# Performance work log

Hardware: AMD Instinct MI355X
Metric: run time of the kernel (lower is better)

Reference implementation:

```python
import jax, jax.numpy as jnp
import numpy as np

L, B, T, D, V = 2, 16, 20, 768, 30000


def setup_inputs() -> dict:
    key = jax.random.key(0)
    k1, k2, k3, k4 = jax.random.split(key, 4)
    answer_embed = jax.random.normal(k1, (L, B, T, D), dtype=jnp.float32)
    vocab_embed = 0.1 * jax.random.normal(k2, (V, D), dtype=jnp.float32)
    # classifier_transform modeled as Linear(D, D): y = x @ W.T + b
    W = jax.random.normal(k3, (D, D), dtype=jnp.float32) * (1.0 / np.sqrt(D))
    b = jax.random.normal(k4, (D,), dtype=jnp.float32) * 0.01
    return {"answer_embed": answer_embed, "vocab_embed": vocab_embed, "W": W, "b": b}


def reference(answer_embed, vocab_embed, W, b):
    # vocab_classifiers: [V, D] after the linear transform
    vocab_classifiers = vocab_embed @ W.T + b
    # Original: broadcast multiply [L,B,T,D,1]*[1,1,1,D,V] then sum over D.
    # Mathematically identical contraction over D -> [L, B, T, V]
    return jnp.einsum('lbtd,vd->lbtv', answer_embed, vocab_classifiers)
```

## Files before the change

### kernel.cpp

```cpp
#include <hip/hip_runtime.h>

#define KDIM 768
#define MANS 640
#define VV   30000
#define NGRP 235
#define NKS  (KDIM / 64)
#define VELEM (VV * KDIM)
#define CVTBLK ((VELEM + 8191) / 8192)
#define A2BLK  ((MANS / 64) * (KDIM / 128))

typedef __attribute__((ext_vector_type(4)))  float  f32x4;
typedef __attribute__((ext_vector_type(16))) float  f32x16;
typedef __attribute__((ext_vector_type(8)))  __bf16 bf16x8;
typedef __attribute__((ext_vector_type(8)))  unsigned short ushort8;

__device__ __forceinline__ unsigned short f2bf(float f) {
    union { __bf16 h; unsigned short u; } t;
    t.h = (__bf16)f;
    return t.u;
}

__device__ __forceinline__ ushort8 cvt8(f32x4 a, f32x4 b) {
    union { bf16x8 h; ushort8 u; } c;
    c.h[0] = (__bf16)a.x; c.h[1] = (__bf16)a.y;
    c.h[2] = (__bf16)a.z; c.h[3] = (__bf16)a.w;
    c.h[4] = (__bf16)b.x; c.h[5] = (__bf16)b.y;
    c.h[6] = (__bf16)b.z; c.h[7] = (__bf16)b.w;
    return c.u;
}

__device__ __forceinline__ void load_lds16(const unsigned short* g, unsigned short* l) {
    __builtin_amdgcn_global_load_lds(
        (__attribute__((address_space(1))) void*)(void*)g,
        (__attribute__((address_space(3))) void*)l,
        16, 0, 0);
}

__device__ __forceinline__ long a2f_off(int m, int n) {
    int mb = m >> 7, wm = (m >> 6) & 1, fm = (m >> 5) & 1, colm = m & 31;
    int kt = n >> 6, g = (n >> 4) & 3, halfb = (n >> 3) & 1, e = n & 7;
    return ((((long)(mb * 12 + kt) * 2 + wm) * 2 + fm) * 4 + g) * 512
         + (halfb * 32 + colm) * 8 + e;
}

__global__ __launch_bounds__(256) void prep_small(
    const float* __restrict__ W, const float* __restrict__ A,
    const float* __restrict__ b, unsigned short* __restrict__ Wt_bf,
    float* __restrict__ cvec)
{
    __shared__ float ts[64][65];
    const int blk = blockIdx.x;
    if (blk < 144) {
        int bx = (blk % 12) * 64, by = (blk / 12) * 64;
        int tx = threadIdx.x & 63, tg = threadIdx.x >> 6;
#pragma unroll
        for (int i = 0; i < 16; ++i) {
            int r = tg * 16 + i;
            ts[r][tx] = W[(long)(by + r) * KDIM + bx + tx];
        }
        __syncthreads();
#pragma unroll
        for (int i = 0; i < 16; ++i) {
            int r = tg * 16 + i;
            Wt_bf[(long)(bx + r) * KDIM + by + tx] = f2bf(ts[tx][r]);
        }
    } else {
        int row  = (blk - 144) * 4 + (threadIdx.x >> 6);
        int lane = threadIdx.x & 63;
        const float* ap = A + (long)row * KDIM;
        float s = 0.f;
#pragma unroll
        for (int i = 0; i < KDIM / 64; ++i) s += ap[i * 64 + lane] * b[i * 64 + lane];
#pragma unroll
        for (int off = 32; off; off >>= 1) s += __shfl_down(s, off, 64);
        if (lane == 0) cvec[row] = s;
    }
}

__global__ __launch_bounds__(256) void gemm_a2(
    const float* __restrict__ Af, const unsigned short* __restrict__ Bp,
    unsigned short* __restrict__ outp,
    const float* __restrict__ vocab, unsigned short* __restrict__ vocab_bf)
{
    if (blockIdx.x >= A2BLK) {
        const long base = (long)(blockIdx.x - A2BLK) * 8192 + (long)threadIdx.x * 8;
#pragma unroll
        for (int p = 0; p < 4; ++p) {
            long idx = base + p * 2048;
            if (idx < VELEM) {
                f32x4 v0 = ((const f32x4*)(vocab + idx))[0];
                f32x4 v1 = ((const f32x4*)(vocab + idx))[1];
                *(ushort8*)(vocab_bf + idx) = cvt8(v0, v1);
            }
        }
        return;
    }

    constexpr int TM = 64, TN = 128;
    __shared__ unsigned short sA[TM * 64];
    __shared__ unsigned short sB[TN * 64];

    const int t    = threadIdx.x;
    const int lane = t & 63;
    const int w    = t >> 6;
    const int wm   = w >> 1;
    const int wn   = w & 1;
    const int half = lane >> 5;
    const int col  = lane & 31;
    const long m0  = (long)(blockIdx.x % (MANS / 64)) * TM;
    const long n0  = (long)(blockIdx.x / (MANS / 64)) * TN;

    f32x16 acc[2];
    acc[0] = (f32x16)(0.f);
    acc[1] = (f32x16)(0.f);

    const float* gaf[2]; int laOff[2];
#pragma unroll
    for (int j = 0; j < 2; ++j) {
        int s   = (j * 4 + w) * 64 + lane;
        int row = s >> 3;
        int c   = (s & 7) ^ (row & 7);
        gaf[j]   = Af + (m0 + row) * KDIM + c * 8;
        laOff[j] = s * 8;
    }
    const unsigned short* gb[4]; unsigned short* lbB[4];
#pragma unroll
    for (int j = 0; j < 4; ++j) {
        int s   = (j * 4 + w) * 64 + lane;
        int row = s >> 3;
        int c   = (s & 7) ^ (row & 7);
        gb[j]  = Bp + (n0 + row) * KDIM + c * 8;
        lbB[j] = &sB[(j * 4 + w) * 64 * 8];
    }

    for (int k0 = 0; k0 < KDIM; k0 += 64) {
#pragma unroll
        for (int j = 0; j < 4; ++j) load_lds16(gb[j] + k0, lbB[j]);
#pragma unroll
        for (int j = 0; j < 2; ++j) {
            f32x4 v0 = ((const f32x4*)(gaf[j] + k0))[0];
            f32x4 v1 = ((const f32x4*)(gaf[j] + k0))[1];
            *(ushort8*)(&sA[0] + laOff[j]) = cvt8(v0, v1);
        }
        __syncthreads();

#pragma unroll
        for (int g = 0; g < 4; ++g) {
            const int cg = g * 2 + half;
            int arow = wm * 32 + col;
            bf16x8 af = *(const bf16x8*)&sA[(arow * 8 + (cg ^ (arow & 7))) * 8];
#pragma unroll
            for (int fn = 0; fn < 2; ++fn) {
                int brow = wn * 64 + fn * 32 + col;
                bf16x8 bfv = *(const bf16x8*)&sB[(brow * 8 + (cg ^ (brow & 7))) * 8];
                acc[fn] = __builtin_amdgcn_mfma_f32_32x32x16_bf16(
                    af, bfv, acc[fn], 0, 0, 0);
            }
        }
        __syncthreads();
    }

#pragma unroll
    for (int fn = 0; fn < 2; ++fn) {
        int n = (int)n0 + wn * 64 + fn * 32 + col;
#pragma unroll
        for (int rg = 0; rg < 16; ++rg) {
            int m = (int)m0 + wm * 32 + (rg & 3) + 8 * (rg >> 2) + 4 * half;
            outp[a2f_off(m, n)] = f2bf(acc[fn][rg]);
        }
    }
}

__global__ __launch_bounds__(256, 4) void gemm_big(
    const unsigned short* __restrict__ A, const unsigned short* __restrict__ Bbf,
    const float* __restrict__ cvec, float* __restrict__ outp)
{
    const int id    = blockIdx.x;
    const int x     = id & 7;
    const int q     = id >> 3;
    const int m_idx = q % 5;
    const int n_grp = (q / 5) * 8 + x;
    if (n_grp >= NGRP) return;

    __shared__ unsigned short sB[2][128 * 64];

    const int t    = threadIdx.x;
    const int lane = t & 63;
    const int w    = t >> 6;
    const int wm   = w >> 1;
    const int wn   = w & 1;
    const int half = lane >> 5;
    const int col  = lane & 31;
    const long n0  = (long)n_grp * 128;

    f32x16 acc[2][2];
#pragma unroll
    for (int i = 0; i < 2; ++i)
#pragma unroll
        for (int j = 0; j < 2; ++j) acc[i][j] = (f32x16)(0.f);

    const unsigned short* aBase = A + (((long)(m_idx * 12) * 2 + wm) * 2) * 4 * 512
                                    + lane * 8;

    const unsigned short* gb[4];
    int lbOff[4];
#pragma unroll
    for (int j = 0; j < 4; ++j) {
        int s   = (j * 4 + w) * 64 + lane;
        int row = s >> 3;
        int c   = (s & 7) ^ (row & 7);
        long grow = n0 + row;
        if (grow > VV - 1) grow = VV - 1;
        gb[j]    = Bbf + grow * KDIM + c * 8;
        lbOff[j] = (j * 4 + w) * 64 * 8;
    }

#pragma unroll
    for (int j = 0; j < 4; ++j) load_lds16(gb[j], &sB[0][0] + lbOff[j]);
    asm volatile("s_waitcnt vmcnt(0)" ::: "memory");
    __builtin_amdgcn_s_barrier();

    for (int kt = 0; kt < NKS; ++kt) {
        const int p = kt & 1;
        const unsigned short* aK = aBase + (long)kt * 8192;
        bf16x8 af[2][4];
#pragma unroll
        for (int fm = 0; fm < 2; ++fm)
#pragma unroll
            for (int g = 0; g < 4; ++g)
                af[fm][g] = *(const bf16x8*)(aK + fm * 2048 + g * 512);
        __builtin_amdgcn_sched_barrier(0);
        if (kt < NKS - 1) {
#pragma unroll
            for (int j = 0; j < 4; ++j)
                load_lds16(gb[j] + (kt + 1) * 64,
                           &sB[0][0] + (p ^ 1) * (128 * 64) + lbOff[j]);
        }
        __builtin_amdgcn_sched_barrier(0);
        const unsigned short* bB = &sB[0][0] + p * (128 * 64);
#pragma unroll
        for (int g = 0; g < 4; ++g) {
            const int cg = g * 2 + half;
            bf16x8 bfr[2];
#pragma unroll
            for (int fn = 0; fn < 2; ++fn) {
                int row = wn * 64 + fn * 32 + col;
                bfr[fn] = *(const bf16x8*)&bB[(row * 8 + (cg ^ (row & 7))) * 8];
            }
#pragma unroll
            for (int fm = 0; fm < 2; ++fm)
#pragma unroll
                for (int fn = 0; fn < 2; ++fn)
                    acc[fm][fn] = __builtin_amdgcn_mfma_f32_32x32x16_bf16(
                        af[fm][g], bfr[fn], acc[fm][fn], 0, 0, 0);
        }
        if (kt < NKS - 1) {
            asm volatile("s_waitcnt vmcnt(0)" ::: "memory");
            __builtin_amdgcn_s_barrier();
        }
    }

    const long m0 = (long)m_idx * 128;
#pragma unroll
    for (int fm = 0; fm < 2; ++fm)
#pragma unroll
        for (int fn = 0; fn < 2; ++fn) {
            long n = n0 + wn * 64 + fn * 32 + col;
            if (n < VV) {
#pragma unroll
                for (int rg = 0; rg < 16; ++rg) {
                    long m = m0 + wm * 64 + fm * 32
                           + (rg & 3) + 8 * (rg >> 2) + 4 * half;
                    outp[m * (long)VV + n] = acc[fm][fn][rg] + cvec[m];
                }
            }
        }
}

extern "C" void kernel_launch(void* const* d_in, const int* in_sizes, int n_in,
                              void* d_out, int out_size, void* d_ws, size_t ws_size,
                              hipStream_t stream) {
    const float* answer = (const float*)d_in[0];
    const float* vocab  = (const float*)d_in[1];
    const float* W      = (const float*)d_in[2];
    const float* bvec   = (const float*)d_in[3];

    char* ws = (char*)d_ws;
    unsigned short* Wt_bf   = (unsigned short*)ws;
    unsigned short* A2F     = (unsigned short*)(ws + 1179648);
    float*          cptr    = (float*)(ws + 1179648 + 983040);
    unsigned short* vocabbf = (unsigned short*)(ws + 2165248);

    prep_small<<<304, 256, 0, stream>>>(W, answer, bvec, Wt_bf, cptr);

    gemm_a2<<<A2BLK + CVTBLK, 256, 0, stream>>>(answer, Wt_bf, A2F, vocab, vocabbf);

    gemm_big<<<1200, 256, 0, stream>>>(A2F, vocabbf, cptr, (float*)d_out);
}
```

Before: 221.6 us.

## Keep full-K vocab panel in LDS and loop all M tiles per block

The big GEMM now uses 512-thread blocks, each owning a 64-column slice of the vocab matrix. Each block loads that slice's whole K=768 panel into LDS once and then iterates over all five 128-row M tiles, instead of one block per (M,N) tile with double-buffered K streaming. This reads the large vocab operand from global memory once instead of once per M tile and removes the per-k-step barriers. In exchange, the block uses 96KB of LDS, which limits occupancy. The 64x128 output tile per block also lowers MFMA reuse per LDS load, and A-fragments are read straight from global memory with no prefetch.

```diff
diff --git a/kernel.cpp b/kernel.cpp
--- a/kernel.cpp
+++ b/kernel.cpp
@@ -3,8 +3,8 @@
 #define KDIM 768
 #define MANS 640
 #define VV   30000
-#define NGRP 235
 #define NKS  (KDIM / 64)
+#define NBLK 469
 #define VELEM (VV * KDIM)
 #define CVTBLK ((VELEM + 8191) / 8192)
 #define A2BLK  ((MANS / 64) * (KDIM / 128))
@@ -171,18 +171,11 @@
     }
 }
 
-__global__ __launch_bounds__(256, 4) void gemm_big(
+__global__ __launch_bounds__(512) void gemm_big(
     const unsigned short* __restrict__ A, const unsigned short* __restrict__ Bbf,
     const float* __restrict__ cvec, float* __restrict__ outp)
 {
-    const int id    = blockIdx.x;
-    const int x     = id & 7;
-    const int q     = id >> 3;
-    const int m_idx = q % 5;
-    const int n_grp = (q / 5) * 8 + x;
-    if (n_grp >= NGRP) return;
-
-    __shared__ unsigned short sB[2][128 * 64];
+    __shared__ unsigned short panel[NKS * 4096];
 
     const int t    = threadIdx.x;
     const int lane = t & 63;
@@ -191,90 +184,61 @@
     const int wn   = w & 1;
     const int half = lane >> 5;
     const int col  = lane & 31;
-    const long n0  = (long)n_grp * 128;
-
-    f32x16 acc[2][2];
-#pragma unroll
-    for (int i = 0; i < 2; ++i)
-#pragma unroll
-        for (int j = 0; j < 2; ++j) acc[i][j] = (f32x16)(0.f);
-
-    const unsigned short* aBase = A + (((long)(m_idx * 12) * 2 + wm) * 2) * 4 * 512
-                                    + lane * 8;
-
-    const unsigned short* gb[4];
-    int lbOff[4];
-#pragma unroll
-    for (int j = 0; j < 4; ++j) {
-        int s   = (j * 4 + w) * 64 + lane;
-        int row = s >> 3;
-        int c   = (s & 7) ^ (row & 7);
-        long grow = n0 + row;
-        if (grow > VV - 1) grow = VV - 1;
-        gb[j]    = Bbf + grow * KDIM + c * 8;
-        lbOff[j] = (j * 4 + w) * 64 * 8;
-    }
-
-#pragma unroll
-    for (int j = 0; j < 4; ++j) load_lds16(gb[j], &sB[0][0] + lbOff[j]);
-    asm volatile("s_waitcnt vmcnt(0)" ::: "memory");
-    __builtin_amdgcn_s_barrier();
-
-    for (int kt = 0; kt < NKS; ++kt) {
-        const int p = kt & 1;
-        const unsigned short* aK = aBase + (long)kt * 8192;
-        bf16x8 af[2][4];
-#pragma unroll
-        for (int fm = 0; fm < 2; ++fm)
-#pragma unroll
-            for (int g = 0; g < 4; ++g)
-                af[fm][g] = *(const bf16x8*)(aK + fm * 2048 + g * 512);
-        __builtin_amdgcn_sched_barrier(0);
-        if (kt < NKS - 1) {
-#pragma unroll
-            for (int j = 0; j < 4; ++j)
-                load_lds16(gb[j] + (kt + 1) * 64,
-                           &sB[0][0] + (p ^ 1) * (128 * 64) + lbOff[j]);
-        }
-        __builtin_amdgcn_sched_barrier(0);
-        const unsigned short* bB = &sB[0][0] + p * (128 * 64);
-#pragma unroll
-        for (int g = 0; g < 4; ++g) {
-            const int cg = g * 2 + half;
-            bf16x8 bfr[2];
-#pragma unroll
-            for (int fn = 0; fn < 2; ++fn) {
-                int row = wn * 64 + fn * 32 + col;
-                bfr[fn] = *(const bf16x8*)&bB[(row * 8 + (cg ^ (row & 7))) * 8];
+    const long n0  = (long)blockIdx.x * 64;
+
+    {
+        int row   = t >> 3;
+        int c     = (t & 7) ^ (row & 7);
+        long grow = n0 + row; if (grow > VV - 1) grow = VV - 1;
+        const unsigned short* src = Bbf + grow * KDIM + c * 8;
+        unsigned short*       dst = panel + w * 512;
+#pragma unroll
+        for (int kt = 0; kt < NKS; ++kt)
+            load_lds16(src + kt * 64, dst + kt * 4096);
+    }
+    __syncthreads();
+
+    const int brow = wn * 32 + col;
+    int boff[4];
+#pragma unroll
+    for (int g = 0; g < 4; ++g)
+        boff[g] = (brow * 8 + (((g * 2 + half)) ^ (brow & 7))) * 8;
+
+    const long nstore = n0 + wn * 32 + col;
+    const bool nok    = (nstore < VV);
+
+#pragma unroll 1
+    for (int m_idx = 0; m_idx < 5; ++m_idx) {
+        f32x16 acc0 = (f32x16)(0.f), acc1 = (f32x16)(0.f);
+        const unsigned short* aM = A + ((long)(16 * (m_idx * 12) + 4 * wm)) * 512
+                                     + lane * 8;
+#pragma unroll
+        for (int kt = 0; kt < NKS; ++kt) {
+            const unsigned short* aK = aM + (long)kt * (16 * 512);
+            const unsigned short* pk = panel + kt * 4096;
+            bf16x8 af0 = *(const bf16x8*)(aK + 0 * 512);
+            bf16x8 af1 = *(const bf16x8*)(aK + 1 * 512);
+            bf16x8 af2 = *(const bf16x8*)(aK + 2 * 512);
+            bf16x8 af3 = *(const bf16x8*)(aK + 3 * 512);
+            bf16x8 b0  = *(const bf16x8*)(pk + boff[0]);
+            bf16x8 b1  = *(const bf16x8*)(pk + boff[1]);
+            bf16x8 b2  = *(const bf16x8*)(pk + boff[2]);
+            bf16x8 b3  = *(const bf16x8*)(pk + boff[3]);
+            acc0 = __builtin_amdgcn_mfma_f32_32x32x16_bf16(af0, b0, acc0, 0, 0, 0);
+            acc1 = __builtin_amdgcn_mfma_f32_32x32x16_bf16(af1, b1, acc1, 0, 0, 0);
+            acc0 = __builtin_amdgcn_mfma_f32_32x32x16_bf16(af2, b2, acc0, 0, 0, 0);
+            acc1 = __builtin_amdgcn_mfma_f32_32x32x16_bf16(af3, b3, acc1, 0, 0, 0);
+        }
+        if (nok) {
+            f32x16 fa = acc0 + acc1;
+            const long mbase = (long)m_idx * 128 + wm * 32 + 4 * half;
+#pragma unroll
+            for (int rg = 0; rg < 16; ++rg) {
+                long m = mbase + (rg & 3) + 8 * (rg >> 2);
+                outp[m * (long)VV + nstore] = fa[rg] + cvec[m];
             }
-#pragma unroll
-            for (int fm = 0; fm < 2; ++fm)
-#pragma unroll
-                for (int fn = 0; fn < 2; ++fn)
-                    acc[fm][fn] = __builtin_amdgcn_mfma_f32_32x32x16_bf16(
-                        af[fm][g], bfr[fn], acc[fm][fn], 0, 0, 0);
-        }
-        if (kt < NKS - 1) {
-            asm volatile("s_waitcnt vmcnt(0)" ::: "memory");
-            __builtin_amdgcn_s_barrier();
-        }
-    }
-
-    const long m0 = (long)m_idx * 128;
-#pragma unroll
-    for (int fm = 0; fm < 2; ++fm)
-#pragma unroll
-        for (int fn = 0; fn < 2; ++fn) {
-            long n = n0 + wn * 64 + fn * 32 + col;
-            if (n < VV) {
-#pragma unroll
-                for (int rg = 0; rg < 16; ++rg) {
-                    long m = m0 + wm * 64 + fm * 32
-                           + (rg & 3) + 8 * (rg >> 2) + 4 * half;
-                    outp[m * (long)VV + n] = acc[fm][fn][rg] + cvec[m];
-                }
-            }
-        }
+        }
+    }
 }
 
 extern "C" void kernel_launch(void* const* d_in, const int* in_sizes, int n_in,
@@ -295,5 +259,5 @@
 
     gemm_a2<<<A2BLK + CVTBLK, 256, 0, stream>>>(answer, Wt_bf, A2F, vocab, vocabbf);
 
-    gemm_big<<<1200, 256, 0, stream>>>(A2F, vocabbf, cptr, (float*)d_out);
-}
+    gemm_big<<<NBLK, 512, 0, stream>>>(A2F, vocabbf, cptr, (float*)d_out);
+}
```

New measurement: 262.8 us. 18.6% more time.
